# Kernel tuning notes

Measured on AMD Instinct MI355X. Metric: run time of the kernel, lower is better.

## Reference

```python
import jax, jax.numpy as jnp
import numpy as np

N, E, G = 50000, 600000, 256
IN_C, EMB, HID, OUT = 64, 128, 128, 36


def _glorot(key, fan_in, fan_out):
    lim = np.sqrt(6.0 / (fan_in + fan_out)).astype(np.float32)
    return jax.random.uniform(key, (fan_in, fan_out), jnp.float32, -lim, lim)


def setup_inputs() -> dict:
    key = jax.random.key(0)
    ks = jax.random.split(key, 12)
    x = jax.random.normal(ks[0], (N, IN_C), jnp.float32)
    edge_index = jax.random.randint(ks[1], (2, E), 0, N, jnp.int64)
    edge_attr = jax.random.uniform(ks[2], (E,), jnp.float32)
    # deterministic sorted batch assignment -> every graph id 0..G-1 is nonempty
    batch = ((jnp.arange(N, dtype=jnp.int64) * G) // N).astype(jnp.int64)
    rho = jax.random.uniform(ks[3], (G,), jnp.float32)
    return {
        "x": x,
        "edge_attr": edge_attr,
        "rho": rho,
        "conv0_w": _glorot(ks[4], IN_C, EMB),
        "conv0_b": jnp.zeros((EMB,), jnp.float32),
        "conv1_w": _glorot(ks[5], EMB, EMB),
        "conv1_b": jnp.zeros((EMB,), jnp.float32),
        "mlp0_w": _glorot(ks[6], 2 * EMB + 1, HID),
        "mlp0_b": jnp.zeros((HID,), jnp.float32),
        "mlp1_w": _glorot(ks[7], HID, HID),
        "mlp1_b": jnp.zeros((HID,), jnp.float32),
        "out_w": _glorot(ks[8], HID, OUT),
        "out_b": jnp.zeros((OUT,), jnp.float32),
        "edge_index": edge_index,
        "batch": batch,
    }


def _gcn_conv(h, row, col, w, W, b):
    # PyG GCNConv: self-loops already appended in (row, col, w).
    deg = jax.ops.segment_sum(w, col, num_segments=N)  # in-degree by edge weight
    dis = jnp.where(deg > 0, jax.lax.rsqrt(jnp.maximum(deg, 1e-30)), 0.0)
    norm = dis[row] * w * dis[col]                     # [E+N]
    h = h @ W                                          # [N, out]
    msg = norm[:, None] * h[row]                       # gather + scale
    return jax.ops.segment_sum(msg, col, num_segments=N) + b


def reference(x, edge_attr, rho, conv0_w, conv0_b, conv1_w, conv1_b,
              mlp0_w, mlp0_b, mlp1_w, mlp1_b, out_w, out_b,
              edge_index, batch):
    # add self-loops with weight 1
    loops = jnp.arange(N, dtype=edge_index.dtype)
    row = jnp.concatenate([edge_index[0], loops])
    col = jnp.concatenate([edge_index[1], loops])
    w = jnp.concatenate([edge_attr, jnp.ones((N,), edge_attr.dtype)])

    h = jax.nn.relu(_gcn_conv(x, row, col, w, conv0_w, conv0_b))
    h = jax.nn.relu(_gcn_conv(h, row, col, w, conv1_w, conv1_b))

    gmp = jax.ops.segment_max(h, batch, num_segments=G)             # [G, EMB]
    cnt = jax.ops.segment_sum(jnp.ones((N,), h.dtype), batch, num_segments=G)
    gap = jax.ops.segment_sum(h, batch, num_segments=G) / cnt[:, None]
    hg = jnp.concatenate([gmp, gap, rho[:, None]], axis=1)          # [G, 2*EMB+1]

    hg = jax.nn.relu(hg @ mlp0_w + mlp0_b)
    hg = jax.nn.relu(hg @ mlp1_w + mlp1_b)
    return hg @ out_w + out_b
```

## Files before the change

kernel.cpp:

```cpp
#include <hip/hip_runtime.h>
#include <hip/hip_fp16.h>
#include <math.h>

using half8 = __attribute__((ext_vector_type(8))) _Float16;
using f32x4 = __attribute__((ext_vector_type(4))) float;

#define CAP 64


__device__ __forceinline__ float wdec(unsigned int v) {
    __half h;
    *reinterpret_cast<unsigned short*>(&h) = (unsigned short)(v >> 16);
    return __half2float(h);
}

__device__ __forceinline__ unsigned int wenc(int src, float w) {
    __half h = __float2half(w);
    return (unsigned int)src |
           ((unsigned int)(*reinterpret_cast<unsigned short*>(&h)) << 16);
}

__device__ __forceinline__ void st_half4(__half* p, float4 v) {
    __half2 a = __floats2half2_rn(v.x, v.y);
    __half2 b = __floats2half2_rn(v.z, v.w);
    int2 raw;
    raw.x = *reinterpret_cast<int*>(&a);
    raw.y = *reinterpret_cast<int*>(&b);
    *reinterpret_cast<int2*>(p) = raw;
}


__global__ void k_setup(const float* __restrict__ w0, __half* __restrict__ wt0,
                        const float* __restrict__ w1, __half* __restrict__ wt1,
                        int* __restrict__ cursor, int n) {
    int i = blockIdx.x * blockDim.x + threadIdx.x;
    if (i < 64 * 128) {
        int k = i >> 7, c = i & 127;
        wt0[c * 64 + k] = __float2half(w0[i]);
    }
    if (i < 128 * 128) {
        int k = i >> 7, c = i & 127;
        wt1[c * 128 + k] = __float2half(w1[i]);
    }
    if (i < n) cursor[i] = 0;
}


__global__ void k_place(const int* __restrict__ row, const int* __restrict__ col,
                        const float* __restrict__ w, int* __restrict__ cursor,
                        unsigned int* __restrict__ slab, int e) {
    int base = (blockIdx.x * blockDim.x + threadIdx.x) * 4;
    if (base + 3 < e) {
        int4 r4 = *reinterpret_cast<const int4*>(&row[base]);
        int4 c4 = *reinterpret_cast<const int4*>(&col[base]);
        float4 w4 = *reinterpret_cast<const float4*>(&w[base]);
        int s0 = atomicAdd(&cursor[c4.x], 1);
        int s1 = atomicAdd(&cursor[c4.y], 1);
        int s2 = atomicAdd(&cursor[c4.z], 1);
        int s3 = atomicAdd(&cursor[c4.w], 1);
        if (s0 < CAP) slab[(size_t)c4.x * CAP + s0] = wenc(r4.x, w4.x);
        if (s1 < CAP) slab[(size_t)c4.y * CAP + s1] = wenc(r4.y, w4.y);
        if (s2 < CAP) slab[(size_t)c4.z * CAP + s2] = wenc(r4.z, w4.z);
        if (s3 < CAP) slab[(size_t)c4.w * CAP + s3] = wenc(r4.w, w4.w);
    } else {
        for (int i = base; i < e; ++i) {
            int c = col[i];
            int s = atomicAdd(&cursor[c], 1);
            if (s < CAP) slab[(size_t)c * CAP + s] = wenc(row[i], w[i]);
        }
    }
}

__global__ __launch_bounds__(256) void k_degscale(
    const unsigned int* __restrict__ slab, const int* __restrict__ cursor,
    const float* __restrict__ x, float* __restrict__ dis,
    __half* __restrict__ xs, int n)
{
    __shared__ float sdis[256];
    int t = threadIdx.x;
    int base = blockIdx.x * 256;
    int i = base + t;
    if (i < n) {
        int cnt = min(cursor[i], CAP);
        float s = 1.0f;
        const unsigned int* p = &slab[(size_t)i * CAP];
        for (int j = 0; j < cnt; ++j) s += wdec(p[j]);
        float d = rsqrtf(s);
        dis[i] = d;
        sdis[t] = d;
    }
    __syncthreads();
#pragma unroll
    for (int it = 0; it < 16; ++it) {
        int id = it * 256 + t;
        int node_l = id >> 4;
        if (base + node_l < n) {
            float d = sdis[node_l];
            float4 v = reinterpret_cast<const float4*>(x)[(size_t)base * 16 + id];
            v.x *= d; v.y *= d; v.z *= d; v.w *= d;
            st_half4(&xs[((size_t)base * 16 + id) * 4], v);
        }
    }
}


template<int K, bool SC>
__global__ __launch_bounds__(256) void k_agg_gemm(
    const __half* __restrict__ hs, const unsigned int* __restrict__ slab,
    const int* __restrict__ cursor, const float* __restrict__ dis,
    const __half* __restrict__ wt, const float* __restrict__ bias,
    __half* __restrict__ out, int n)
{
    constexpr int SA = K + 8;
    constexpr int CPR = K / 8;
    constexpr int CW = K / 4;
    __shared__ _Float16 Al[64 * SA];
    __shared__ _Float16 Wl[128 * SA];
    const int tid = threadIdx.x;
    const int row0 = blockIdx.x * 64;

#pragma unroll
    for (int it = 0; it < (128 * CPR) / 256; ++it) {
        int id = tid + it * 256;
        int c = id / CPR, kc = id % CPR;
        int4 raw = *reinterpret_cast<const int4*>(&wt[(size_t)c * K + kc * 8]);
        *reinterpret_cast<int4*>(&Wl[c * SA + kc * 8]) = raw;
    }

    {
        const int lr = tid >> 2, part = tid & 3;
        const int node = row0 + lr;
        const int c0 = part * CW;
        if (node < n) {
            float acc[CW];
#pragma unroll
            for (int cc = 0; cc < CW / 8; ++cc) {
                half8 v = *reinterpret_cast<const half8*>(&hs[(size_t)node * K + c0 + cc * 8]);
#pragma unroll
                for (int u = 0; u < 8; ++u) acc[cc * 8 + u] = (float)v[u];
            }
            int cnt = min(cursor[node], CAP);
            const unsigned int* sp = &slab[(size_t)node * CAP];
            for (int j = 0; j < cnt; ++j) {
                unsigned int rec = sp[j];
                int src = rec & 0xFFFF;
                float w = wdec(rec);
#pragma unroll
                for (int cc = 0; cc < CW / 8; ++cc) {
                    half8 v = *reinterpret_cast<const half8*>(&hs[(size_t)src * K + c0 + cc * 8]);
#pragma unroll
                    for (int u = 0; u < 8; ++u)
                        acc[cc * 8 + u] = fmaf(w, (float)v[u], acc[cc * 8 + u]);
                }
            }
            float d = dis[node];
#pragma unroll
            for (int cc = 0; cc < CW / 8; ++cc) {
                half8 hv;
#pragma unroll
                for (int u = 0; u < 8; ++u) hv[u] = (_Float16)(d * acc[cc * 8 + u]);
                *reinterpret_cast<half8*>(&Al[lr * SA + c0 + cc * 8]) = hv;
            }
        }
    }
    __syncthreads();

    const int l = tid & 63, w = tid >> 6;
    const int r = l & 15, kg = l >> 4;

    f32x4 acc[8];
#pragma unroll
    for (int ct = 0; ct < 8; ++ct) acc[ct] = (f32x4){0.f, 0.f, 0.f, 0.f};

#pragma unroll
    for (int kst = 0; kst < K / 32; ++kst) {
        half8 af = *reinterpret_cast<const half8*>(&Al[(16 * w + r) * SA + kst * 32 + kg * 8]);
#pragma unroll
        for (int ct = 0; ct < 8; ++ct) {
            half8 bf = *reinterpret_cast<const half8*>(&Wl[(16 * ct + r) * SA + kst * 32 + kg * 8]);
            acc[ct] = __builtin_amdgcn_mfma_f32_16x16x32_f16(af, bf, acc[ct], 0, 0, 0);
        }
    }

    float sc[4];
#pragma unroll
    for (int q = 0; q < 4; ++q) {
        int gr = row0 + 16 * w + kg * 4 + q;
        sc[q] = (SC && gr < n) ? dis[gr] : 1.0f;
    }
#pragma unroll
    for (int ct = 0; ct < 8; ++ct) {
        float bv = bias[16 * ct + r];
#pragma unroll
        for (int q = 0; q < 4; ++q) {
            int gr = row0 + 16 * w + kg * 4 + q;
            if (gr < n) {
                float v = fmaxf(acc[ct][q] + bv, 0.f);
                if constexpr (SC) v *= sc[q];
                out[(size_t)gr * 128 + 16 * ct + r] = __float2half(v);
            }
        }
    }
}


__device__ __forceinline__ int lowbound(const int* __restrict__ b, int n, int key) {
    int lo = 0, hi = n;
    while (lo < hi) { int mid = (lo + hi) >> 1; if (b[mid] < key) lo = mid + 1; else hi = mid; }
    return lo;
}

#define NSLICE 8

__global__ __launch_bounds__(128) void k_pool_part(
    const __half* __restrict__ h, const int* __restrict__ batch,
    float* __restrict__ part, int n)
{
    int g = blockIdx.x >> 3, s = blockIdx.x & (NSLICE - 1);
    int ch = threadIdx.x;
    __shared__ int sbeg, send;
    if (ch == 0) {
        sbeg = lowbound(batch, n, g);
        send = lowbound(batch, n, g + 1);
    }
    __syncthreads();
    float mx = -INFINITY, sm = 0.f;
    for (int i = sbeg + s; i < send; i += NSLICE) {
        float v = __half2float(h[(size_t)i * 128 + ch]);
        mx = fmaxf(mx, v);
        sm += v;
    }
    size_t base = ((size_t)g * NSLICE + s) * 256;
    part[base + ch] = mx;
    part[base + 128 + ch] = sm;
}


__global__ __launch_bounds__(256) void k_head_mlp(
    const float* __restrict__ part, const int* __restrict__ batch,
    const float* __restrict__ rho,
    const float* __restrict__ w0, const float* __restrict__ b0,
    const float* __restrict__ w1, const float* __restrict__ b1,
    const float* __restrict__ w2, const float* __restrict__ b2,
    float* __restrict__ out, int n)
{
    int g = blockIdx.x;
    int tid = threadIdx.x;
    int ch = tid & 127, half = tid >> 7;
    __shared__ float hg[257];
    __shared__ float t0[128];
    __shared__ float red[2][128];
    __shared__ int scnt;
    if (tid == 0) {
        int beg = lowbound(batch, n, g);
        int end = lowbound(batch, n, g + 1);
        scnt = end - beg;
        hg[256] = rho[g];
    }
    {
        float mx = -INFINITY, sm = 0.f;
        for (int s = half * (NSLICE / 2); s < (half + 1) * (NSLICE / 2); ++s) {
            size_t base = ((size_t)g * NSLICE + s) * 256;
            mx = fmaxf(mx, part[base + ch]);
            sm += part[base + 128 + ch];
        }
        red[half][ch] = mx;
        __syncthreads();
        if (half == 0) {
            float m2 = fmaxf(mx, red[1][ch]);
            hg[ch] = m2;
            red[0][ch] = sm;
        }
        __syncthreads();
        if (half == 1) red[1][ch] = sm + red[0][ch];
        __syncthreads();
        if (half == 0) hg[128 + ch] = red[1][ch] / (float)scnt;
        __syncthreads();
    }
    {
        float a = 0.f, b = 0.f;
        int j0 = half * 128;
        int jend = half ? 257 : 128;
        int j = j0;
        for (; j + 2 <= jend; j += 2) {
            a = fmaf(hg[j], w0[(size_t)j * 128 + ch], a);
            b = fmaf(hg[j + 1], w0[(size_t)(j + 1) * 128 + ch], b);
        }
        if (j < jend) a = fmaf(hg[j], w0[(size_t)j * 128 + ch], a);
        red[half][ch] = a + b;
        __syncthreads();
        if (half == 0) t0[ch] = fmaxf(red[0][ch] + red[1][ch] + b0[ch], 0.f);
        __syncthreads();
    }
    {
        float a = 0.f, b = 0.f;
        int j0 = half * 64;
        for (int j = j0; j < j0 + 64; j += 2) {
            a = fmaf(t0[j], w1[(size_t)j * 128 + ch], a);
            b = fmaf(t0[j + 1], w1[(size_t)(j + 1) * 128 + ch], b);
        }
        red[half][ch] = a + b;
        __syncthreads();
        if (half == 0) hg[ch] = fmaxf(red[0][ch] + red[1][ch] + b1[ch], 0.f);
        __syncthreads();
    }
    if (ch < 36) {
        float a = 0.f, b = 0.f;
        int j0 = half * 64;
        for (int j = j0; j < j0 + 64; j += 2) {
            a = fmaf(hg[j], w2[(size_t)j * 36 + ch], a);
            b = fmaf(hg[j + 1], w2[(size_t)(j + 1) * 36 + ch], b);
        }
        red[half][ch] = a + b;
    }
    __syncthreads();
    if (half == 0 && ch < 36)
        out[(size_t)g * 36 + ch] = red[0][ch] + red[1][ch] + b2[ch];
}


extern "C" void kernel_launch(void* const* d_in, const int* in_sizes, int n_in,
                              void* d_out, int out_size, void* d_ws, size_t ws_size,
                              hipStream_t stream)
{
    const float* x        = (const float*)d_in[0];
    const float* edge_attr= (const float*)d_in[1];
    const float* rho      = (const float*)d_in[2];
    const float* conv0_w  = (const float*)d_in[3];
    const float* conv0_b  = (const float*)d_in[4];
    const float* conv1_w  = (const float*)d_in[5];
    const float* conv1_b  = (const float*)d_in[6];
    const float* mlp0_w   = (const float*)d_in[7];
    const float* mlp0_b   = (const float*)d_in[8];
    const float* mlp1_w   = (const float*)d_in[9];
    const float* mlp1_b   = (const float*)d_in[10];
    const float* out_w    = (const float*)d_in[11];
    const float* out_b    = (const float*)d_in[12];
    const int*   edge_idx = (const int*)d_in[13];
    const int*   batch    = (const int*)d_in[14];

    const int N = in_sizes[0] / 64;
    const int E = in_sizes[1];
    const int G = in_sizes[2];
    const int* erow = edge_idx;
    const int* ecol = edge_idx + E;

    char* ws = (char*)d_ws;
    size_t off = 0;
    auto alloc = [&](size_t bytes) -> void* {
        off = (off + 255) & ~(size_t)255;
        void* p = ws + off;
        off += bytes;
        return p;
    };
    float*        dis    = (float*)alloc((size_t)N * 4);
    int*          cursor = (int*)  alloc((size_t)N * 4);
    unsigned int* slab   = (unsigned int*)alloc((size_t)N * CAP * 4);
    __half*       bufA   = (__half*)alloc((size_t)N * 128 * 2);
    __half*       bufB   = (__half*)alloc((size_t)N * 128 * 2);
    float*        part   = (float*)alloc((size_t)G * NSLICE * 256 * 4);
    __half*       wt0    = (__half*)alloc((size_t)64 * 128 * 2);
    __half*       wt1    = (__half*)alloc((size_t)128 * 128 * 2);

    dim3 b256(256);
    int setup_n = (N > 128 * 128) ? N : 128 * 128;
    k_setup<<<(setup_n + 255) / 256, b256, 0, stream>>>(conv0_w, wt0, conv1_w, wt1, cursor, N);
    k_place<<<((E + 3) / 4 + 255) / 256, b256, 0, stream>>>(erow, ecol, edge_attr, cursor, slab, E);
    k_degscale<<<(N + 255) / 256, b256, 0, stream>>>(slab, cursor, x, dis, bufA, N);

    k_agg_gemm<64, true><<<(N + 63) / 64, b256, 0, stream>>>(bufA, slab, cursor, dis, wt0, conv0_b, bufB, N);
    k_agg_gemm<128, false><<<(N + 63) / 64, b256, 0, stream>>>(bufB, slab, cursor, dis, wt1, conv1_b, bufA, N);

    k_pool_part<<<G * NSLICE, dim3(128), 0, stream>>>(bufA, batch, part, N);
    k_head_mlp<<<G, b256, 0, stream>>>(part, batch, rho,
                                       mlp0_w, mlp0_b, mlp1_w, mlp1_b, out_w, out_b,
                                       (float*)d_out, N);
}
```

Baseline: 166.6 us.

## Split fused aggregate-GEMM into separate wide-parallel gather and MFMA GEMM kernels

Splits each GCN layer's fused aggregation+GEMM kernel into a standalone gather kernel and a separate MFMA GEMM kernel. In the gather kernel each node is handled by 16 or 32 lanes that each own 4 columns, and edge records are read four at a time with uint4 loads. This gives more threads per node and more coalesced row gathers than the old 4 threads per node with long serial loops. The cost is an extra round trip of the aggregated features through global memory and two extra kernel launches. The degree sum in k_degscale is also vectorized with uint4 loads.

```diff
diff --git a/kernel.cpp b/kernel.cpp
--- a/kernel.cpp
+++ b/kernel.cpp
@@ -18,6 +18,13 @@
     __half h = __float2half(w);
     return (unsigned int)src |
            ((unsigned int)(*reinterpret_cast<unsigned short*>(&h)) << 16);
+}
+
+__device__ __forceinline__ float4 ld_half4(const __half* p) {
+    int2 raw = *reinterpret_cast<const int2*>(p);
+    __half2 a = *reinterpret_cast<__half2*>(&raw.x);
+    __half2 b = *reinterpret_cast<__half2*>(&raw.y);
+    return make_float4(__low2float(a), __high2float(a), __low2float(b), __high2float(b));
 }
 
 __device__ __forceinline__ void st_half4(__half* p, float4 v) {
@@ -84,7 +91,12 @@
         int cnt = min(cursor[i], CAP);
         float s = 1.0f;
         const unsigned int* p = &slab[(size_t)i * CAP];
-        for (int j = 0; j < cnt; ++j) s += wdec(p[j]);
+        int j = 0;
+        for (; j + 4 <= cnt; j += 4) {
+            uint4 rec = *reinterpret_cast<const uint4*>(&p[j]);
+            s += wdec(rec.x) + wdec(rec.y) + wdec(rec.z) + wdec(rec.w);
+        }
+        for (; j < cnt; ++j) s += wdec(p[j]);
         float d = rsqrtf(s);
         dis[i] = d;
         sdis[t] = d;
@@ -104,21 +116,71 @@
 }
 
 
-template<int K, bool SC>
-__global__ __launch_bounds__(256) void k_agg_gemm(
+template<int COLS, int LPN>
+__global__ __launch_bounds__(256) void k_agg(
     const __half* __restrict__ hs, const unsigned int* __restrict__ slab,
     const int* __restrict__ cursor, const float* __restrict__ dis,
-    const __half* __restrict__ wt, const float* __restrict__ bias,
+    __half* __restrict__ out, int n)
+{
+    int t = blockIdx.x * blockDim.x + threadIdx.x;
+    int node = t / LPN, lane = t % LPN;
+    if (node >= n) return;
+    int c4 = lane * 4;
+    float4 acc = ld_half4(&hs[(size_t)node * COLS + c4]);
+    int cnt = min(cursor[node], CAP);
+    const unsigned int* sp = &slab[(size_t)node * CAP];
+    int p = 0;
+    for (; p + 4 <= cnt; p += 4) {
+        uint4 rec = *reinterpret_cast<const uint4*>(&sp[p]);
+        float w0 = wdec(rec.x), w1 = wdec(rec.y), w2 = wdec(rec.z), w3 = wdec(rec.w);
+        float4 v0 = ld_half4(&hs[(size_t)(rec.x & 0xFFFF) * COLS + c4]);
+        float4 v1 = ld_half4(&hs[(size_t)(rec.y & 0xFFFF) * COLS + c4]);
+        float4 v2 = ld_half4(&hs[(size_t)(rec.z & 0xFFFF) * COLS + c4]);
+        float4 v3 = ld_half4(&hs[(size_t)(rec.w & 0xFFFF) * COLS + c4]);
+        acc.x = fmaf(w0, v0.x, acc.x); acc.y = fmaf(w0, v0.y, acc.y);
+        acc.z = fmaf(w0, v0.z, acc.z); acc.w = fmaf(w0, v0.w, acc.w);
+        acc.x = fmaf(w1, v1.x, acc.x); acc.y = fmaf(w1, v1.y, acc.y);
+        acc.z = fmaf(w1, v1.z, acc.z); acc.w = fmaf(w1, v1.w, acc.w);
+        acc.x = fmaf(w2, v2.x, acc.x); acc.y = fmaf(w2, v2.y, acc.y);
+        acc.z = fmaf(w2, v2.z, acc.z); acc.w = fmaf(w2, v2.w, acc.w);
+        acc.x = fmaf(w3, v3.x, acc.x); acc.y = fmaf(w3, v3.y, acc.y);
+        acc.z = fmaf(w3, v3.z, acc.z); acc.w = fmaf(w3, v3.w, acc.w);
+    }
+    for (; p < cnt; ++p) {
+        unsigned int rec = sp[p];
+        float w0 = wdec(rec);
+        float4 v0 = ld_half4(&hs[(size_t)(rec & 0xFFFF) * COLS + c4]);
+        acc.x = fmaf(w0, v0.x, acc.x); acc.y = fmaf(w0, v0.y, acc.y);
+        acc.z = fmaf(w0, v0.z, acc.z); acc.w = fmaf(w0, v0.w, acc.w);
+    }
+    float d = dis[node];
+    float4 o;
+    o.x = d * acc.x; o.y = d * acc.y; o.z = d * acc.z; o.w = d * acc.w;
+    st_half4(&out[(size_t)node * COLS + c4], o);
+}
+
+
+template<int K, bool SC>
+__global__ __launch_bounds__(256) void k_gemm_mfma(
+    const __half* __restrict__ A, const __half* __restrict__ wt,
+    const float* __restrict__ bias, const float* __restrict__ scale,
     __half* __restrict__ out, int n)
 {
     constexpr int SA = K + 8;
     constexpr int CPR = K / 8;
-    constexpr int CW = K / 4;
     __shared__ _Float16 Al[64 * SA];
     __shared__ _Float16 Wl[128 * SA];
     const int tid = threadIdx.x;
     const int row0 = blockIdx.x * 64;
 
+#pragma unroll
+    for (int it = 0; it < (64 * CPR) / 256; ++it) {
+        int id = tid + it * 256;
+        int r = id / CPR, kc = id % CPR;
+        int gr = row0 + r; if (gr >= n) gr = n - 1;
+        int4 raw = *reinterpret_cast<const int4*>(&A[(size_t)gr * K + kc * 8]);
+        *reinterpret_cast<int4*>(&Al[r * SA + kc * 8]) = raw;
+    }
 #pragma unroll
     for (int it = 0; it < (128 * CPR) / 256; ++it) {
         int id = tid + it * 256;
@@ -126,43 +188,6 @@
         int4 raw = *reinterpret_cast<const int4*>(&wt[(size_t)c * K + kc * 8]);
         *reinterpret_cast<int4*>(&Wl[c * SA + kc * 8]) = raw;
     }
-
-    {
-        const int lr = tid >> 2, part = tid & 3;
-        const int node = row0 + lr;
-        const int c0 = part * CW;
-        if (node < n) {
-            float acc[CW];
-#pragma unroll
-            for (int cc = 0; cc < CW / 8; ++cc) {
-                half8 v = *reinterpret_cast<const half8*>(&hs[(size_t)node * K + c0 + cc * 8]);
-#pragma unroll
-                for (int u = 0; u < 8; ++u) acc[cc * 8 + u] = (float)v[u];
-            }
-            int cnt = min(cursor[node], CAP);
-            const unsigned int* sp = &slab[(size_t)node * CAP];
-            for (int j = 0; j < cnt; ++j) {
-                unsigned int rec = sp[j];
-                int src = rec & 0xFFFF;
-                float w = wdec(rec);
-#pragma unroll
-                for (int cc = 0; cc < CW / 8; ++cc) {
-                    half8 v = *reinterpret_cast<const half8*>(&hs[(size_t)src * K + c0 + cc * 8]);
-#pragma unroll
-                    for (int u = 0; u < 8; ++u)
-                        acc[cc * 8 + u] = fmaf(w, (float)v[u], acc[cc * 8 + u]);
-                }
-            }
-            float d = dis[node];
-#pragma unroll
-            for (int cc = 0; cc < CW / 8; ++cc) {
-                half8 hv;
-#pragma unroll
-                for (int u = 0; u < 8; ++u) hv[u] = (_Float16)(d * acc[cc * 8 + u]);
-                *reinterpret_cast<half8*>(&Al[lr * SA + c0 + cc * 8]) = hv;
-            }
-        }
-    }
     __syncthreads();
 
     const int l = tid & 63, w = tid >> 6;
@@ -186,7 +211,7 @@
 #pragma unroll
     for (int q = 0; q < 4; ++q) {
         int gr = row0 + 16 * w + kg * 4 + q;
-        sc[q] = (SC && gr < n) ? dis[gr] : 1.0f;
+        sc[q] = (SC && gr < n) ? scale[gr] : 1.0f;
     }
 #pragma unroll
     for (int ct = 0; ct < 8; ++ct) {
@@ -368,8 +393,10 @@
     k_place<<<((E + 3) / 4 + 255) / 256, b256, 0, stream>>>(erow, ecol, edge_attr, cursor, slab, E);
     k_degscale<<<(N + 255) / 256, b256, 0, stream>>>(slab, cursor, x, dis, bufA, N);
 
-    k_agg_gemm<64, true><<<(N + 63) / 64, b256, 0, stream>>>(bufA, slab, cursor, dis, wt0, conv0_b, bufB, N);
-    k_agg_gemm<128, false><<<(N + 63) / 64, b256, 0, stream>>>(bufB, slab, cursor, dis, wt1, conv1_b, bufA, N);
+    k_agg<64, 16><<<((size_t)N * 16 + 255) / 256, b256, 0, stream>>>(bufA, slab, cursor, dis, bufB, N);
+    k_gemm_mfma<64, true><<<(N + 63) / 64, b256, 0, stream>>>(bufB, wt0, conv0_b, dis, bufA, N);
+    k_agg<128, 32><<<((size_t)N * 32 + 255) / 256, b256, 0, stream>>>(bufA, slab, cursor, dis, bufB, N);
+    k_gemm_mfma<128, false><<<(N + 63) / 64, b256, 0, stream>>>(bufB, wt1, conv1_b, nullptr, bufA, N);
 
     k_pool_part<<<G * NSLICE, dim3(128), 0, stream>>>(bufA, batch, part, N);
     k_head_mlp<<<G, b256, 0, stream>>>(part, batch, rho,
```

After: 164.7 us. Within noise of the previous version (-1.2%).
